# Kernel optimization log

Measured on AMD Instinct MI355X. Metric: run time of the kernel, lower is better.

## Reference

```python
import jax, jax.numpy as jnp
import numpy as np

EPS = 1e-6

def _avgpool(x, k):
    # AvgPool2d(kernel_size=k, stride=k) for divisible H, W
    B, C, H, W = x.shape
    return x.reshape(B, C, H // k, k, W // k, k).mean(axis=(3, 5))

def setup_inputs() -> dict:
    key = jax.random.key(0)
    ks = jax.random.split(key, 5)
    B, C, H, W, kern = 32, 128, 32, 32, 2
    shp = (B, C, H, W)
    return {
        "mu_a_": jax.random.normal(ks[0], shp, dtype=jnp.float32),
        "logvar_a_": jax.random.normal(ks[1], shp, dtype=jnp.float32),
        "mu_b_": jax.random.normal(ks[2], shp, dtype=jnp.float32),
        "logvar_b_": jax.random.normal(ks[3], shp, dtype=jnp.float32),
        "eps": jax.random.normal(ks[4], (B, C, H // kern, W // kern), dtype=jnp.float32),
        "kern": kern,
    }

def _log_mean_density(z, mu, var):
    # z: [B,C,h,w] (one MC sample per batch row i); mu/var: [B,C,h,w]
    # pairwise unnormalized Gaussian density ratio, mean over the mixture (j) axis
    d = jnp.exp(-(z[:, None] - mu[None]) ** 2 / (2.0 * var[None])) / jnp.sqrt(var[None])  # [B,B,C,h,w]
    return jnp.log(jnp.mean(d, axis=1) + EPS)  # [B,C,h,w]

def reference(mu_a_, logvar_a_, mu_b_, logvar_b_, eps, kern):
    k = int(kern)
    mu_a = _avgpool(mu_a_, k)
    mu_b = _avgpool(mu_b_, k)
    var_a = _avgpool(jnp.exp(logvar_a_), k) / (k * k)
    var_b = _avgpool(jnp.exp(logvar_b_), k) / (k * k)
    z = mu_a + jnp.sqrt(var_a) * eps  # reparameterized MC samples, one per row
    term = _log_mean_density(z, mu_a, var_a) - _log_mean_density(z, mu_b, var_b)  # [B,C,h,w]
    # torch loop adds each per-i term (shape [C,h,w]) broadcast into a [B,C,h,w]
    # accumulator, then sums -> equals B * sum_i,c,h,w term
    B = mu_a.shape[0]
    return jnp.asarray(B, term.dtype) * jnp.sum(term)
```

## Files before the change

### kernel.cpp

```cpp
#include <hip/hip_runtime.h>


#define GKL_EPS 1e-6f

__global__ __launch_bounds__(256) void gkl_main(
    const float* __restrict__ muA, const float* __restrict__ lvA,
    const float* __restrict__ muB, const float* __restrict__ lvB,
    const float* __restrict__ eps, double* __restrict__ ws)
{
    __shared__ float sh[2720];
    __shared__ float wsum[4];

    const int bid = blockIdx.x;
    const int c   = bid >> 5;
    const int h   = (bid >> 1) & 15;
    const int wh  = bid & 1;
    const int t   = threadIdx.x;
    const int b   = t >> 3;
    const int wl  = t & 7;
    const int w   = wh*8 + wl;

    {
        const int base = ((b*128 + c)*32 + 2*h)*32 + 2*w;

        float2 m0 = *(const float2*)(muA + base);
        float2 m1 = *(const float2*)(muA + base + 32);
        float2 l0 = *(const float2*)(lvA + base);
        float2 l1 = *(const float2*)(lvA + base + 32);
        float2 n0 = *(const float2*)(muB + base);
        float2 n1 = *(const float2*)(muB + base + 32);
        float2 k0 = *(const float2*)(lvB + base);
        float2 k1 = *(const float2*)(lvB + base + 32);
        float ev  = eps[((b*128 + c)*16 + h)*16 + w];

        float mu  = (m0.x + m0.y + m1.x + m1.y) * 0.25f;
        float var = (__expf(l0.x)+__expf(l0.y)+__expf(l1.x)+__expf(l1.y)) * 0.0625f;
        float rs  = __builtin_amdgcn_rsqf(var);
        *(float2*)(sh + wl*68 + 2*b) = make_float2(mu, 0.84932185f * rs);
        sh[2176 + b*17 + wl] = fmaf(var * rs, ev, mu);

        float mub  = (n0.x + n0.y + n1.x + n1.y) * 0.25f;
        float varb = (__expf(k0.x)+__expf(k0.y)+__expf(k1.x)+__expf(k1.y)) * 0.0625f;
        float rsb  = __builtin_amdgcn_rsqf(varb);
        *(float2*)(sh + 1092 + wl*68 + 2*b) = make_float2(mub, 0.84932185f * rsb);
    }
    __syncthreads();

    const int lane = t & 63;
    const int wv   = t >> 6;
    const int i    = lane & 31;
    const int side = lane >> 5;
    const float* __restrict__ qp0 = sh + side*1092 + (wv*2)*68;
    const float* __restrict__ qp1 = qp0 + 68;
    const float z0 = sh[2176 + i*17 + wv*2];
    const float z1 = sh[2176 + i*17 + wv*2 + 1];

    float acc0 = 0.f, acc1 = 0.f;
    #pragma unroll
    for (int k = 0; k < 16; ++k) {
        float4 f = *(const float4*)(qp0 + 4*k);
        float4 g = *(const float4*)(qp1 + 4*k);
        float d0 = z0 - f.x, e0 = d0 * f.y;
        acc0 = fmaf(f.y, exp2f(-(e0*e0)), acc0);
        float d1 = z0 - f.z, e1 = d1 * f.w;
        acc0 = fmaf(f.w, exp2f(-(e1*e1)), acc0);
        float d2 = z1 - g.x, e2 = d2 * g.y;
        acc1 = fmaf(g.y, exp2f(-(e2*e2)), acc1);
        float d3 = z1 - g.z, e3 = d3 * g.w;
        acc1 = fmaf(g.w, exp2f(-(e3*e3)), acc1);
    }
    float lg = __logf(fmaf(acc0, 0.036794063f, GKL_EPS))
             + __logf(fmaf(acc1, 0.036794063f, GKL_EPS));
    float tot = side ? -lg : lg;

    #pragma unroll
    for (int o = 32; o; o >>= 1) tot += __shfl_xor(tot, o, 64);
    if (lane == 0) wsum[wv] = tot;
    __syncthreads();
    if (t == 0)
        ws[bid] = (double)wsum[0] + (double)wsum[1] + (double)wsum[2] + (double)wsum[3];
}

__global__ __launch_bounds__(256) void gkl_final(
    const double* __restrict__ ws, float* __restrict__ out)
{
    __shared__ double part[4];
    const int t = threadIdx.x;
    double s = 0.0;
    for (int k = t; k < 4096; k += 256) s += ws[k];
    #pragma unroll
    for (int o = 32; o; o >>= 1) s += __shfl_xor(s, o, 64);
    if ((t & 63) == 0) part[t >> 6] = s;
    __syncthreads();
    if (t == 0) out[0] = (float)(32.0 * (part[0] + part[1] + part[2] + part[3]));
}

extern "C" void kernel_launch(void* const* d_in, const int* in_sizes, int n_in,
                              void* d_out, int out_size, void* d_ws, size_t ws_size,
                              hipStream_t stream) {
    const float* muA = (const float*)d_in[0];
    const float* lvA = (const float*)d_in[1];
    const float* muB = (const float*)d_in[2];
    const float* lvB = (const float*)d_in[3];
    const float* ep  = (const float*)d_in[4];
    double* ws = (double*)d_ws;
    float* out = (float*)d_out;

    gkl_main<<<4096, 256, 0, stream>>>(muA, lvA, muB, lvB, ep, ws);
    gkl_final<<<1, 256, 0, stream>>>(ws, out);
}
```

Baseline: 122.0 us.

## Process two tiles per block with prefetch and double-buffered shared memory

```diff
diff --git a/kernel.cpp b/kernel.cpp
--- a/kernel.cpp
+++ b/kernel.cpp
@@ -2,83 +2,102 @@
 
 
 #define GKL_EPS 1e-6f
+#define BUFW 1648
+
+struct TR { float2 m0, m1, l0, l1, n0, n1, k0, k1; float ev; };
+
+__device__ __forceinline__ void tile_load(TR& r,
+    const float* __restrict__ muA, const float* __restrict__ lvA,
+    const float* __restrict__ muB, const float* __restrict__ lvB,
+    const float* __restrict__ eps, int b, int c, int h, int w)
+{
+    const int base = ((b*128 + c)*32 + 2*h)*32 + 2*w;
+    r.m0 = *(const float2*)(muA + base);
+    r.m1 = *(const float2*)(muA + base + 32);
+    r.l0 = *(const float2*)(lvA + base);
+    r.l1 = *(const float2*)(lvA + base + 32);
+    r.n0 = *(const float2*)(muB + base);
+    r.n1 = *(const float2*)(muB + base + 32);
+    r.k0 = *(const float2*)(lvB + base);
+    r.k1 = *(const float2*)(lvB + base + 32);
+    r.ev = eps[((b*128 + c)*16 + h)*16 + w];
+}
+
+__device__ __forceinline__ void tile_params(const TR& r, float* shb, int b, int wl)
+{
+    float mu  = (r.m0.x + r.m0.y + r.m1.x + r.m1.y) * 0.25f;
+    float var = (__expf(r.l0.x)+__expf(r.l0.y)+__expf(r.l1.x)+__expf(r.l1.y)) * 0.0625f;
+    float rs  = __builtin_amdgcn_rsqf(var);
+    float s   = 0.84932185f * rs;
+    *(float2*)(shb + wl*68 + 2*b) = make_float2(s, s*mu);
+    shb[1096 + b*17 + wl] = fmaf(var*rs, r.ev, mu);
+
+    float mub  = (r.n0.x + r.n0.y + r.n1.x + r.n1.y) * 0.25f;
+    float varb = (__expf(r.k0.x)+__expf(r.k0.y)+__expf(r.k1.x)+__expf(r.k1.y)) * 0.0625f;
+    float rsb  = __builtin_amdgcn_rsqf(varb);
+    float sb   = 0.84932185f * rsb;
+    *(float2*)(shb + 548 + wl*68 + 2*b) = make_float2(sb, sb*mub);
+}
+
+__device__ __forceinline__ float tile_phase2(const float* shb, int lane, int wv)
+{
+    const int i    = lane & 31;
+    const int side = lane >> 5;
+    const float* qp0 = shb + side*548 + (2*wv)*68;
+    const float* qp1 = qp0 + 68;
+    const float z0 = shb[1096 + i*17 + 2*wv];
+    const float z1 = shb[1096 + i*17 + 2*wv + 1];
+    float acc0 = 0.f, acc1 = 0.f;
+    #pragma unroll
+    for (int k = 0; k < 16; ++k) {
+        float4 f = *(const float4*)(qp0 + 4*k);
+        float4 g = *(const float4*)(qp1 + 4*k);
+        float e0 = fmaf(z0, f.x, -f.y); acc0 = fmaf(f.x, exp2f(-(e0*e0)), acc0);
+        float e1 = fmaf(z0, f.z, -f.w); acc0 = fmaf(f.z, exp2f(-(e1*e1)), acc0);
+        float e2 = fmaf(z1, g.x, -g.y); acc1 = fmaf(g.x, exp2f(-(e2*e2)), acc1);
+        float e3 = fmaf(z1, g.z, -g.w); acc1 = fmaf(g.z, exp2f(-(e3*e3)), acc1);
+    }
+    float lg = __logf(fmaf(acc0, 0.036794063f, GKL_EPS))
+             + __logf(fmaf(acc1, 0.036794063f, GKL_EPS));
+    return side ? -lg : lg;
+}
 
 __global__ __launch_bounds__(256) void gkl_main(
     const float* __restrict__ muA, const float* __restrict__ lvA,
     const float* __restrict__ muB, const float* __restrict__ lvB,
     const float* __restrict__ eps, double* __restrict__ ws)
 {
-    __shared__ float sh[2720];
-    __shared__ float wsum[4];
+    __shared__ float sh[2*BUFW];
 
-    const int bid = blockIdx.x;
-    const int c   = bid >> 5;
-    const int h   = (bid >> 1) & 15;
-    const int wh  = bid & 1;
-    const int t   = threadIdx.x;
-    const int b   = t >> 3;
-    const int wl  = t & 7;
-    const int w   = wh*8 + wl;
+    const int bid  = blockIdx.x;
+    const int t    = threadIdx.x;
+    const int b    = t >> 3;
+    const int wl   = t & 7;
+    const int lane = t & 63;
+    const int wv   = t >> 6;
 
-    {
-        const int base = ((b*128 + c)*32 + 2*h)*32 + 2*w;
+    const int T0 = bid, T1 = bid + 2048;
+    const int c0 = T0 >> 5, h0 = (T0 >> 1) & 15, w0 = (T0 & 1)*8 + wl;
+    const int c1 = T1 >> 5, h1 = (T1 >> 1) & 15, w1 = (T1 & 1)*8 + wl;
 
-        float2 m0 = *(const float2*)(muA + base);
-        float2 m1 = *(const float2*)(muA + base + 32);
-        float2 l0 = *(const float2*)(lvA + base);
-        float2 l1 = *(const float2*)(lvA + base + 32);
-        float2 n0 = *(const float2*)(muB + base);
-        float2 n1 = *(const float2*)(muB + base + 32);
-        float2 k0 = *(const float2*)(lvB + base);
-        float2 k1 = *(const float2*)(lvB + base + 32);
-        float ev  = eps[((b*128 + c)*16 + h)*16 + w];
-
-        float mu  = (m0.x + m0.y + m1.x + m1.y) * 0.25f;
-        float var = (__expf(l0.x)+__expf(l0.y)+__expf(l1.x)+__expf(l1.y)) * 0.0625f;
-        float rs  = __builtin_amdgcn_rsqf(var);
-        *(float2*)(sh + wl*68 + 2*b) = make_float2(mu, 0.84932185f * rs);
-        sh[2176 + b*17 + wl] = fmaf(var * rs, ev, mu);
-
-        float mub  = (n0.x + n0.y + n1.x + n1.y) * 0.25f;
-        float varb = (__expf(k0.x)+__expf(k0.y)+__expf(k1.x)+__expf(k1.y)) * 0.0625f;
-        float rsb  = __builtin_amdgcn_rsqf(varb);
-        *(float2*)(sh + 1092 + wl*68 + 2*b) = make_float2(mub, 0.84932185f * rsb);
-    }
+    TR r0, r1;
+    tile_load(r0, muA, lvA, muB, lvB, eps, b, c0, h0, w0);
+    tile_params(r0, sh, b, wl);
+    tile_load(r1, muA, lvA, muB, lvB, eps, b, c1, h1, w1);
     __syncthreads();
 
-    const int lane = t & 63;
-    const int wv   = t >> 6;
-    const int i    = lane & 31;
-    const int side = lane >> 5;
-    const float* __restrict__ qp0 = sh + side*1092 + (wv*2)*68;
-    const float* __restrict__ qp1 = qp0 + 68;
-    const float z0 = sh[2176 + i*17 + wv*2];
-    const float z1 = sh[2176 + i*17 + wv*2 + 1];
+    float p0 = tile_phase2(sh, lane, wv);
+    #pragma unroll
+    for (int o = 32; o; o >>= 1) p0 += __shfl_xor(p0, o, 64);
+    if (lane == 0) ws[T0*4 + wv] = (double)p0;
 
-    float acc0 = 0.f, acc1 = 0.f;
+    tile_params(r1, sh + BUFW, b, wl);
+    __syncthreads();
+
+    float p1 = tile_phase2(sh + BUFW, lane, wv);
     #pragma unroll
-    for (int k = 0; k < 16; ++k) {
-        float4 f = *(const float4*)(qp0 + 4*k);
-        float4 g = *(const float4*)(qp1 + 4*k);
-        float d0 = z0 - f.x, e0 = d0 * f.y;
-        acc0 = fmaf(f.y, exp2f(-(e0*e0)), acc0);
-        float d1 = z0 - f.z, e1 = d1 * f.w;
-        acc0 = fmaf(f.w, exp2f(-(e1*e1)), acc0);
-        float d2 = z1 - g.x, e2 = d2 * g.y;
-        acc1 = fmaf(g.y, exp2f(-(e2*e2)), acc1);
-        float d3 = z1 - g.z, e3 = d3 * g.w;
-        acc1 = fmaf(g.w, exp2f(-(e3*e3)), acc1);
-    }
-    float lg = __logf(fmaf(acc0, 0.036794063f, GKL_EPS))
-             + __logf(fmaf(acc1, 0.036794063f, GKL_EPS));
-    float tot = side ? -lg : lg;
-
-    #pragma unroll
-    for (int o = 32; o; o >>= 1) tot += __shfl_xor(tot, o, 64);
-    if (lane == 0) wsum[wv] = tot;
-    __syncthreads();
-    if (t == 0)
-        ws[bid] = (double)wsum[0] + (double)wsum[1] + (double)wsum[2] + (double)wsum[3];
+    for (int o = 32; o; o >>= 1) p1 += __shfl_xor(p1, o, 64);
+    if (lane == 0) ws[T1*4 + wv] = (double)p1;
 }
 
 __global__ __launch_bounds__(256) void gkl_final(
@@ -87,7 +106,7 @@
     __shared__ double part[4];
     const int t = threadIdx.x;
     double s = 0.0;
-    for (int k = t; k < 4096; k += 256) s += ws[k];
+    for (int k = t; k < 16384; k += 256) s += ws[k];
     #pragma unroll
     for (int o = 32; o; o >>= 1) s += __shfl_xor(s, o, 64);
     if ((t & 63) == 0) part[t >> 6] = s;
@@ -106,6 +125,6 @@
     double* ws = (double*)d_ws;
     float* out = (float*)d_out;
 
-    gkl_main<<<4096, 256, 0, stream>>>(muA, lvA, muB, lvB, ep, ws);
+    gkl_main<<<2048, 256, 0, stream>>>(muA, lvA, muB, lvB, ep, ws);
     gkl_final<<<1, 256, 0, stream>>>(ws, out);
 }
```

After: 133.6 us. 1.1x slower.
